# Kernel optimization log

Measured on AMD Instinct MI355X. Metric: run time of the kernel, lower is better.

Reference implementation:

```python
import jax, jax.numpy as jnp
import numpy as np

TOP_K = 2


def setup_inputs() -> dict:
    key = jax.random.key(0)
    k1, k2, k3 = jax.random.split(key, 3)
    inp = jax.random.normal(k1, (16384, 2048), dtype=jnp.float32)
    W = jax.random.normal(k2, (64, 2048), dtype=jnp.float32) * 0.02
    b = jax.random.normal(k3, (64,), dtype=jnp.float32) * 0.02
    return {"inp": inp, "W": W, "b": b}


def reference(inp, W, b):
    # gate logits: [tokens, num_expert]
    gate = jnp.einsum("td,ed->te", inp, W) + b
    # top-k over experts (lax.top_k returns sorted; torch used sorted=False,
    # so results match up to a per-token permutation of the k slots)
    top_val, top_idx = jax.lax.top_k(gate, TOP_K)  # [tokens, k]
    gate_score = jax.nn.softmax(top_val, axis=-1)[:, None, :]  # [tokens, 1, k]
    gate_top_k_idx = top_idx.reshape(-1)  # [tokens * k]
    return (gate_top_k_idx, gate_score)
```

## Files before the change

kernel.cpp:

```cpp
#include <hip/hip_runtime.h>
#include <math.h>


#define KDIM 2048
#define NEXP 64
#define TPB  256
#define BK   16
#define LDST (BK + 4)

__global__ __launch_bounds__(256) void transpose_w_kernel(
    const float* __restrict__ W, float* __restrict__ Wt)
{
    const int idx = blockIdx.x * 256 + threadIdx.x;
    const int e = idx >> 11;
    const int k = idx & 2047;
    Wt[k * NEXP + e] = W[idx];
}

__global__ __launch_bounds__(256)
__attribute__((amdgpu_waves_per_eu(2, 4)))
void gate_partial_kernel(
    const float* __restrict__ inp,
    const float* __restrict__ Wt,
    float* __restrict__ partial,
    int tokens, int kPerSplit)
{
    __shared__ float As[TPB * LDST];

    const int tid     = threadIdx.x;
    const int tokBase = blockIdx.x * TPB;
    const int split   = blockIdx.y;
    const int k0      = split * kPerSplit;

    const int srow = tid >> 2;
    const int scol = (tid & 3) << 2;
    const float* aBase = inp + (size_t)tokBase * KDIM + k0;

    float4 stage[4];
    #pragma unroll
    for (int p = 0; p < 4; ++p)
        stage[p] = *(const float4*)(aBase + (size_t)(srow + 64 * p) * KDIM + scol);

    float acc[NEXP];
    #pragma unroll
    for (int e = 0; e < NEXP; ++e) acc[e] = 0.0f;

    const int NT = kPerSplit / BK;
    for (int kt = 0; kt < NT; ++kt) {
        __syncthreads();
        #pragma unroll
        for (int p = 0; p < 4; ++p)
            *(float4*)&As[(srow + 64 * p) * LDST + scol] = stage[p];
        __syncthreads();
        if (kt + 1 < NT) {
            const int koff = (kt + 1) * BK;
            #pragma unroll
            for (int p = 0; p < 4; ++p)
                stage[p] = *(const float4*)(aBase + (size_t)(srow + 64 * p) * KDIM + koff + scol);
        }
        const float* __restrict__ wTile = Wt + (size_t)(k0 + kt * BK) * NEXP;
        #pragma unroll
        for (int kq = 0; kq < BK / 4; ++kq) {
            const float4 a4 = *(const float4*)&As[tid * LDST + (kq << 2)];
            #pragma unroll
            for (int j = 0; j < 4; ++j) {
                const float a = (j == 0) ? a4.x : (j == 1) ? a4.y : (j == 2) ? a4.z : a4.w;
                const float* __restrict__ wr = wTile + ((kq << 2) + j) * NEXP;
                #pragma unroll
                for (int e = 0; e < NEXP; ++e)
                    acc[e] = fmaf(a, wr[e], acc[e]);
            }
        }
    }

    float* p = partial + ((size_t)split * tokens + tokBase + tid) * NEXP;
    #pragma unroll
    for (int e = 0; e < NEXP; e += 4)
        *(float4*)&p[e] = make_float4(acc[e], acc[e + 1], acc[e + 2], acc[e + 3]);
}

__global__ __launch_bounds__(256) void reduce_topk_kernel(
    const float* __restrict__ partial,
    const float* __restrict__ bias,
    float* __restrict__ out,
    int tokens, int S)
{
    const int tid = threadIdx.x;
    const int tx  = tid & 15;
    const int ty  = tid >> 4;
    const int token = blockIdx.x * 16 + ty;
    const int eBase = tx << 2;

    float4 v = make_float4(0.f, 0.f, 0.f, 0.f);
    for (int s = 0; s < S; ++s) {
        const float4 p = *(const float4*)&partial[((size_t)s * tokens + token) * NEXP + eBase];
        v.x += p.x; v.y += p.y; v.z += p.z; v.w += p.w;
    }
    const float4 bv = *(const float4*)&bias[eBase];
    float g[4] = { v.x + bv.x, v.y + bv.y, v.z + bv.z, v.w + bv.w };

    float v1 = g[0]; int i1 = eBase;
    float v2 = -INFINITY; int i2 = -1;
    #pragma unroll
    for (int c = 1; c < 4; ++c) {
        const float vv = g[c];
        const int   ii = eBase + c;
        if (vv > v1)      { v2 = v1; i2 = i1; v1 = vv; i1 = ii; }
        else if (vv > v2) { v2 = vv; i2 = ii; }
    }
    #pragma unroll
    for (int m = 1; m <= 8; m <<= 1) {
        const float ov1 = __shfl_xor(v1, m);
        const int   oi1 = __shfl_xor(i1, m);
        const float ov2 = __shfl_xor(v2, m);
        const int   oi2 = __shfl_xor(i2, m);
        const bool aw = (v1 > ov1) || (v1 == ov1 && i1 < oi1);
        const float nv1 = aw ? v1  : ov1;  const int ni1 = aw ? i1  : oi1;
        const float lv  = aw ? ov1 : v1;   const int li  = aw ? oi1 : i1;
        const float sv  = aw ? v2  : ov2;  const int si  = aw ? i2  : oi2;
        const bool sw = (sv > lv) || (sv == lv && si < li);
        v1 = nv1; i1 = ni1;
        v2 = sw ? sv : lv; i2 = sw ? si : li;
    }
    if (tx == 0) {
        const float e2 = expf(v2 - v1);
        const float denom = 1.0f + e2;
        out[2 * token]     = (float)i1;
        out[2 * token + 1] = (float)i2;
        out[tokens * 2 + 2 * token]     = 1.0f / denom;
        out[tokens * 2 + 2 * token + 1] = e2 / denom;
    }
}

extern "C" void kernel_launch(void* const* d_in, const int* in_sizes, int n_in,
                              void* d_out, int out_size, void* d_ws, size_t ws_size,
                              hipStream_t stream) {
    const float* inp  = (const float*)d_in[0];
    const float* W    = (const float*)d_in[1];
    const float* bias = (const float*)d_in[2];
    float* out = (float*)d_out;

    const int tokens = in_sizes[0] / KDIM;

    int S = 16;
    while (S > 1 &&
           (size_t)S * tokens * NEXP * sizeof(float) + (size_t)KDIM * NEXP * sizeof(float) > ws_size)
        S >>= 1;
    const int kPerSplit = KDIM / S;

    float* partial = (float*)d_ws;
    float* Wt = partial + (size_t)S * tokens * NEXP;

    transpose_w_kernel<<<(NEXP * KDIM) / 256, 256, 0, stream>>>(W, Wt);

    dim3 grid(tokens / TPB, S);
    gate_partial_kernel<<<grid, 256, 0, stream>>>(inp, Wt, partial, tokens, kPerSplit);

    reduce_topk_kernel<<<tokens / 16, 256, 0, stream>>>(partial, bias, out, tokens, S);
}
```

Measured before the change: 265.0 us.

## Register-block gate GEMM as 16x8 outer-product tiles with W staged in LDS

Restructures the partial GEMM so each thread computes a 16-token by 8-expert register tile instead of one token times all 64 experts. A-tiles are stored transposed (k-major) in LDS with padding gaps, and W tiles are also staged into LDS rather than read from global/scalar memory each iteration. The block now covers 512 tokens with BK=8, so each LDS value is reused across many FMAs. This trades register pressure (occupancy capped at 2 waves/EU) and scalar stores into LDS for fewer memory ops per FMA.

```diff
diff --git a/kernel.cpp b/kernel.cpp
--- a/kernel.cpp
+++ b/kernel.cpp
@@ -4,9 +4,12 @@
 
 #define KDIM 2048
 #define NEXP 64
-#define TPB  256
-#define BK   16
-#define LDST (BK + 4)
+#define BTOK 512
+#define BK   8
+#define AROW 640
+#define WROW 68
+
+__device__ __forceinline__ int cgap(int t) { return t + ((t >> 4) << 2); }
 
 __global__ __launch_bounds__(256) void transpose_w_kernel(
     const float* __restrict__ W, float* __restrict__ Wt)
@@ -18,65 +21,93 @@
 }
 
 __global__ __launch_bounds__(256)
-__attribute__((amdgpu_waves_per_eu(2, 4)))
+__attribute__((amdgpu_waves_per_eu(2, 2)))
 void gate_partial_kernel(
     const float* __restrict__ inp,
     const float* __restrict__ Wt,
     float* __restrict__ partial,
     int tokens, int kPerSplit)
 {
-    __shared__ float As[TPB * LDST];
+    __shared__ float As[BK * AROW];
+    __shared__ float Ws[BK * WROW];
 
     const int tid     = threadIdx.x;
-    const int tokBase = blockIdx.x * TPB;
+    const int tx      = tid & 7;
+    const int tg      = tid >> 3;
+    const int tokBase = blockIdx.x * BTOK;
     const int split   = blockIdx.y;
-    const int k0      = split * kPerSplit;
+    const int k0g     = split * kPerSplit;
 
-    const int srow = tid >> 2;
-    const int scol = (tid & 3) << 2;
-    const float* aBase = inp + (size_t)tokBase * KDIM + k0;
+    const int st  = tid >> 2;
+    const int sk  = (tid & 3) << 2;
+    const int st2 = tid >> 1;
+    const int sk2 = (tid & 1) << 2;
+    const float* aBase = inp + (size_t)tokBase * KDIM + k0g;
+
+    const int wi = tid << 1;
+    const int wk = wi >> 6;
+    const int we = wi & 63;
 
     float4 stage[4];
+    float2 wstage;
     #pragma unroll
     for (int p = 0; p < 4; ++p)
-        stage[p] = *(const float4*)(aBase + (size_t)(srow + 64 * p) * KDIM + scol);
+        stage[p] = *(const float4*)(aBase + (size_t)(st2 + 128 * p) * KDIM + sk2);
+    wstage = *(const float2*)(Wt + (size_t)(k0g + wk) * NEXP + we);
 
-    float acc[NEXP];
+    float acc[16][8];
     #pragma unroll
-    for (int e = 0; e < NEXP; ++e) acc[e] = 0.0f;
+    for (int i = 0; i < 16; ++i)
+        #pragma unroll
+        for (int j = 0; j < 8; ++j) acc[i][j] = 0.0f;
 
     const int NT = kPerSplit / BK;
+    const int ctg = tg * 20;
     for (int kt = 0; kt < NT; ++kt) {
         __syncthreads();
         #pragma unroll
-        for (int p = 0; p < 4; ++p)
-            *(float4*)&As[(srow + 64 * p) * LDST + scol] = stage[p];
+        for (int p = 0; p < 4; ++p) {
+            const int t = st2 + 128 * p;
+            const int ct = cgap(t);
+            #pragma unroll
+            for (int c = 0; c < 4; ++c)
+                As[(sk2 + c) * AROW + ct] = ((const float*)&stage[p])[c];
+        }
+        *(float2*)&Ws[wk * WROW + we] = wstage;
         __syncthreads();
         if (kt + 1 < NT) {
             const int koff = (kt + 1) * BK;
             #pragma unroll
             for (int p = 0; p < 4; ++p)
-                stage[p] = *(const float4*)(aBase + (size_t)(srow + 64 * p) * KDIM + koff + scol);
+                stage[p] = *(const float4*)(aBase + (size_t)(st2 + 128 * p) * KDIM + koff + sk2);
+            wstage = *(const float2*)(Wt + (size_t)(k0g + koff + wk) * NEXP + we);
         }
-        const float* __restrict__ wTile = Wt + (size_t)(k0 + kt * BK) * NEXP;
         #pragma unroll
-        for (int kq = 0; kq < BK / 4; ++kq) {
-            const float4 a4 = *(const float4*)&As[tid * LDST + (kq << 2)];
+        for (int k = 0; k < BK; ++k) {
+            float4 a0 = *(const float4*)&As[k * AROW + ctg];
+            float4 a1 = *(const float4*)&As[k * AROW + ctg + 4];
+            float4 a2 = *(const float4*)&As[k * AROW + ctg + 8];
+            float4 a3 = *(const float4*)&As[k * AROW + ctg + 12];
+            float4 w0 = *(const float4*)&Ws[k * WROW + tx * 8];
+            float4 w1 = *(const float4*)&Ws[k * WROW + tx * 8 + 4];
+            const float a[16] = { a0.x,a0.y,a0.z,a0.w, a1.x,a1.y,a1.z,a1.w,
+                                  a2.x,a2.y,a2.z,a2.w, a3.x,a3.y,a3.z,a3.w };
+            const float w[8]  = { w0.x,w0.y,w0.z,w0.w, w1.x,w1.y,w1.z,w1.w };
             #pragma unroll
-            for (int j = 0; j < 4; ++j) {
-                const float a = (j == 0) ? a4.x : (j == 1) ? a4.y : (j == 2) ? a4.z : a4.w;
-                const float* __restrict__ wr = wTile + ((kq << 2) + j) * NEXP;
+            for (int i = 0; i < 16; ++i)
                 #pragma unroll
-                for (int e = 0; e < NEXP; ++e)
-                    acc[e] = fmaf(a, wr[e], acc[e]);
-            }
+                for (int j = 0; j < 8; ++j)
+                    acc[i][j] = fmaf(a[i], w[j], acc[i][j]);
         }
     }
 
-    float* p = partial + ((size_t)split * tokens + tokBase + tid) * NEXP;
     #pragma unroll
-    for (int e = 0; e < NEXP; e += 4)
-        *(float4*)&p[e] = make_float4(acc[e], acc[e + 1], acc[e + 2], acc[e + 3]);
+    for (int i = 0; i < 16; ++i) {
+        const int token = tokBase + tg * 16 + i;
+        float* p = partial + ((size_t)split * tokens + token) * NEXP + tx * 8;
+        *(float4*)&p[0] = make_float4(acc[i][0], acc[i][1], acc[i][2], acc[i][3]);
+        *(float4*)&p[4] = make_float4(acc[i][4], acc[i][5], acc[i][6], acc[i][7]);
+    }
 }
 
 __global__ __launch_bounds__(256) void reduce_topk_kernel(
@@ -153,7 +184,7 @@
 
     transpose_w_kernel<<<(NEXP * KDIM) / 256, 256, 0, stream>>>(W, Wt);
 
-    dim3 grid(tokens / TPB, S);
+    dim3 grid(tokens / BTOK, S);
     gate_partial_kernel<<<grid, 256, 0, stream>>>(inp, Wt, partial, tokens, kPerSplit);
 
     reduce_topk_kernel<<<tokens / 16, 256, 0, stream>>>(partial, bias, out, tokens, S);
```

After: 521.5 us. +96.8%, slower.
